# Optimization experiments

Hardware: AMD Instinct MI355X
Metric: run time of the kernel (lower is better)

Reference implementation:

```python
import jax, jax.numpy as jnp
import numpy as np

B, T, HID = 2, 2048, 1536
H, HKV, D = 12, 2, 128
EPS = 1e-6
NEG = -1e9


def setup_inputs() -> dict:
    key = jax.random.key(0)
    ks = jax.random.split(key, 8)
    # rotary embeddings built from real angles (cos/sin of position*inv_freq)
    inv_freq = 1.0 / (10000.0 ** (jnp.arange(0, D, 2, dtype=jnp.float32) / D))  # [D/2]
    pos = jnp.arange(T, dtype=jnp.float32)
    ang = pos[:, None] * inv_freq[None, :]                       # [T, D/2]
    emb = jnp.concatenate([ang, ang], axis=-1)                   # [T, D]
    cos = jnp.broadcast_to(jnp.cos(emb)[None], (B, T, D))
    sin = jnp.broadcast_to(jnp.sin(emb)[None], (B, T, D))
    # additive causal mask [1,1,T,T]
    causal = jnp.tril(jnp.ones((T, T), dtype=bool))
    attention_mask = jnp.where(causal, 0.0, NEG).astype(jnp.float32)[None, None]
    s = 0.02
    return {
        "hidden_states": jax.random.normal(ks[0], (B, T, HID), jnp.float32),
        "cos": cos,
        "sin": sin,
        "attention_mask": attention_mask,
        "q_w": jax.random.normal(ks[1], (H * D, HID), jnp.float32) * s,
        "k_w": jax.random.normal(ks[2], (HKV * D, HID), jnp.float32) * s,
        "v_w": jax.random.normal(ks[3], (HKV * D, HID), jnp.float32) * s,
        "o_w": jax.random.normal(ks[4], (HID, H * D), jnp.float32) * s,
        "q_norm_w": jnp.ones((D,), jnp.float32),
        "k_norm_w": jnp.ones((D,), jnp.float32),
    }


def _rms_norm(x, w):
    # per-head RMSNorm over last dim (head_dim), computed in fp32
    xf = x.astype(jnp.float32)
    var = jnp.mean(xf * xf, axis=-1, keepdims=True)
    return (w * (xf * jax.lax.rsqrt(var + EPS))).astype(x.dtype)


def _rotate_half(x):
    x1, x2 = jnp.split(x, 2, axis=-1)
    return jnp.concatenate([-x2, x1], axis=-1)


def reference(hidden_states, cos, sin, attention_mask, q_w, k_w, v_w, o_w, q_norm_w, k_norm_w):
    b, t, _ = hidden_states.shape
    n_rep = H // HKV
    scale = D ** -0.5

    # projections -> [B, n_heads, T, D]
    q = (hidden_states @ q_w.T).reshape(b, t, H, D)
    k = (hidden_states @ k_w.T).reshape(b, t, HKV, D)
    v = (hidden_states @ v_w.T).reshape(b, t, HKV, D).transpose(0, 2, 1, 3)

    # per-head QK RMSNorm, then to [B, H, T, D]
    q = _rms_norm(q, q_norm_w).transpose(0, 2, 1, 3)
    k = _rms_norm(k, k_norm_w).transpose(0, 2, 1, 3)

    # RoPE (cos/sin broadcast over head axis)
    c = cos[:, None, :, :]
    s = sin[:, None, :, :]
    q = q * c + _rotate_half(q) * s
    k = k * c + _rotate_half(k) * s

    # GQA repeat_kv: [B, HKV, T, D] -> [B, H, T, D]
    k = jnp.repeat(k, n_rep, axis=1)
    v = jnp.repeat(v, n_rep, axis=1)

    attn = jnp.einsum('bhqd,bhkd->bhqk', q, k) * scale + attention_mask
    attn = jax.nn.softmax(attn.astype(jnp.float32), axis=-1).astype(q.dtype)
    out = jnp.einsum('bhqk,bhkd->bhqd', attn, v)
    out = out.transpose(0, 2, 1, 3).reshape(b, t, H * D)
    return out @ o_w.T
```

## Files before the change

kernel.cpp:

```cpp
#include <hip/hip_runtime.h>
#include <hip/hip_bf16.h>


#define B_   2
#define T_   2048
#define HID_ 1536
#define H_   12
#define HKV_ 2
#define D_   128
#define GQ_  (H_ / HKV_)
#define NQKV_ 2048
#define SCALE_ 0.08838834764831845f

typedef unsigned short u16;
typedef __attribute__((ext_vector_type(4))) float f32x4;
typedef __attribute__((ext_vector_type(8))) short bf16x8;
typedef __attribute__((ext_vector_type(4))) unsigned short u16x4;
typedef __attribute__((ext_vector_type(8))) unsigned short u16x8;

__device__ __forceinline__ u16 f2b(float f) {
  union { __hip_bfloat16 h; u16 u; } cv;
  cv.h = __float2bfloat16(f);
  return cv.u;
}
__device__ __forceinline__ float b2f(u16 u) {
  union { float f; unsigned i; } cv;
  cv.i = ((unsigned)u) << 16;
  return cv.f;
}

__device__ __forceinline__ void glds16(const u16* g, u16* l) {
  __builtin_amdgcn_global_load_lds((const __attribute__((address_space(1))) void*)g,
                                   (__attribute__((address_space(3))) void*)l, 16, 0, 0);
}

__global__ __launch_bounds__(256) void cvt_f32_bf16(const float* __restrict__ src,
                                                    u16* __restrict__ dst, int n4) {
  int i = blockIdx.x * 256 + threadIdx.x;
  const int stride = gridDim.x * 256;
  for (; i < n4; i += stride) {
    const float4 v = reinterpret_cast<const float4*>(src)[i];
    u16x4 o = {f2b(v.x), f2b(v.y), f2b(v.z), f2b(v.w)};
    reinterpret_cast<u16x4*>(dst)[i] = o;
  }
}

__device__ __forceinline__ void cstore(float* p, float v) { *p = v; }
__device__ __forceinline__ void cstore(u16* p, float v) { *p = f2b(v); }

template <typename CT>
__global__ __launch_bounds__(256) void gemm_bt(const u16* __restrict__ A,
                                               const u16* __restrict__ W,
                                               CT* __restrict__ C,
                                               int M, int N, int K) {
  __shared__ __align__(16) u16 As[128 * 32];
  __shared__ __align__(16) u16 Ws[128 * 32];
  const int tid  = threadIdx.x;
  const int lane = tid & 63;
  const int wid  = tid >> 6;
  const int wr = wid >> 1, wc = wid & 1;
  const int l15 = lane & 15, kg = lane >> 4;
  const int rowBase = blockIdx.y * 128;
  const int colBase = blockIdx.x * 128;

  const int srow = lane >> 2;
  const int scol = (lane & 3) << 3;
  const u16* Ab = A + (size_t)(rowBase + wid * 16 + srow) * K + scol;
  const u16* Wb = W + (size_t)(colBase + wid * 16 + srow) * K + scol;
  u16* AsW = &As[wid * 512];
  u16* WsW = &Ws[wid * 512];

  const f32x4 zero4 = {0.f, 0.f, 0.f, 0.f};
  f32x4 acc[4][4];
#pragma unroll
  for (int m = 0; m < 4; ++m)
#pragma unroll
    for (int n = 0; n < 4; ++n) acc[m][n] = zero4;

  for (int k0 = 0; k0 < K; k0 += 32) {
    __syncthreads();
    glds16(Ab + k0, AsW);
    glds16(Ab + (size_t)64 * K + k0, AsW + 2048);
    glds16(Wb + k0, WsW);
    glds16(Wb + (size_t)64 * K + k0, WsW + 2048);
    __syncthreads();
    bf16x8 a[4], b[4];
#pragma unroll
    for (int m = 0; m < 4; ++m)
      a[m] = *reinterpret_cast<const bf16x8*>(&As[(wr * 64 + m * 16 + l15) * 32 + kg * 8]);
#pragma unroll
    for (int n = 0; n < 4; ++n)
      b[n] = *reinterpret_cast<const bf16x8*>(&Ws[(wc * 64 + n * 16 + l15) * 32 + kg * 8]);
#pragma unroll
    for (int m = 0; m < 4; ++m)
#pragma unroll
      for (int n = 0; n < 4; ++n)
        acc[m][n] = __builtin_amdgcn_mfma_f32_16x16x32_bf16(a[m], b[n], acc[m][n], 0, 0, 0);
  }
#pragma unroll
  for (int m = 0; m < 4; ++m) {
    const int row0 = rowBase + wr * 64 + m * 16 + kg * 4;
#pragma unroll
    for (int n = 0; n < 4; ++n) {
      const int col = colBase + wc * 64 + n * 16 + l15;
#pragma unroll
      for (int r = 0; r < 4; ++r) cstore(&C[(size_t)(row0 + r) * N + col], acc[m][n][r]);
    }
  }
}

__global__ __launch_bounds__(256) void norm_rope_cvt(
    const u16* __restrict__ qkv, const float* __restrict__ cosb,
    const float* __restrict__ sinb, const float* __restrict__ q_nw,
    const float* __restrict__ k_nw, u16* __restrict__ q_b,
    u16* __restrict__ k_b, u16* __restrict__ vt_b) {
  const int gwave = (int)((blockIdx.x * 256 + threadIdx.x) >> 6);
  const int lane = threadIdx.x & 63;
  const int NQ = B_ * T_ * H_;
  const int NK = B_ * T_ * HKV_;
  if (gwave < NQ) {
    const int bt = gwave / H_, h = gwave - bt * H_;
    const u16* src = qkv + (size_t)bt * NQKV_ + h * D_;
    const float x1 = b2f(src[lane]), x2 = b2f(src[lane + 64]);
    float ss = x1 * x1 + x2 * x2;
#pragma unroll
    for (int m = 32; m >= 1; m >>= 1) ss += __shfl_xor(ss, m);
    const float rinv = rsqrtf(ss * (1.0f / D_) + 1e-6f);
    const float c1 = cosb[(size_t)bt * D_ + lane], c2 = cosb[(size_t)bt * D_ + lane + 64];
    const float s1 = sinb[(size_t)bt * D_ + lane], s2 = sinb[(size_t)bt * D_ + lane + 64];
    const float n1 = x1 * rinv * q_nw[lane], n2 = x2 * rinv * q_nw[lane + 64];
    const float o1 = (n1 * c1 - n2 * s1) * SCALE_;
    const float o2 = (n2 * c2 + n1 * s2) * SCALE_;
    const int b = bt >> 11, t = bt & (T_ - 1);
    u16* dst = q_b + ((size_t)(b * H_ + h) * T_ + t) * D_;
    dst[lane] = f2b(o1);
    dst[lane + 64] = f2b(o2);
  } else if (gwave < NQ + NK) {
    const int r = gwave - NQ;
    const int bt = r >> 1, hv = r & 1;
    const u16* src = qkv + (size_t)bt * NQKV_ + 1536 + hv * D_;
    const float x1 = b2f(src[lane]), x2 = b2f(src[lane + 64]);
    float ss = x1 * x1 + x2 * x2;
#pragma unroll
    for (int m = 32; m >= 1; m >>= 1) ss += __shfl_xor(ss, m);
    const float rinv = rsqrtf(ss * (1.0f / D_) + 1e-6f);
    const float c1 = cosb[(size_t)bt * D_ + lane], c2 = cosb[(size_t)bt * D_ + lane + 64];
    const float s1 = sinb[(size_t)bt * D_ + lane], s2 = sinb[(size_t)bt * D_ + lane + 64];
    const float n1 = x1 * rinv * k_nw[lane], n2 = x2 * rinv * k_nw[lane + 64];
    const float o1 = n1 * c1 - n2 * s1;
    const float o2 = n2 * c2 + n1 * s2;
    const int b = bt >> 11, t = bt & (T_ - 1);
    u16* dst = k_b + ((size_t)(b * HKV_ + hv) * T_ + t) * D_;
    dst[lane] = f2b(o1);
    dst[lane + 64] = f2b(o2);
  } else {
    const int r = gwave - NQ - NK;
    const int bt = r >> 1, hv = r & 1;
    const u16* src = qkv + (size_t)bt * NQKV_ + 1792 + hv * D_;
    const float x1 = b2f(src[lane]), x2 = b2f(src[lane + 64]);
    const int b = bt >> 11, t = bt & (T_ - 1);
    const int kk = t & 63;
    const int tp = (t & ~63) | (kk & 32) | (((kk >> 2) & 3) << 3) |
                   (((kk >> 4) & 1) << 2) | (kk & 3);
    u16* dst = vt_b + (size_t)(b * HKV_ + hv) * D_ * T_;
    dst[(size_t)lane * T_ + tp] = f2b(x1);
    dst[(size_t)(lane + 64) * T_ + tp] = f2b(x2);
  }
}

__global__ __launch_bounds__(256) void attn_kernel(const u16* __restrict__ q_b,
                                                   const u16* __restrict__ k_b,
                                                   const u16* __restrict__ vt_b,
                                                   u16* __restrict__ aout,
                                                   u16* __restrict__ po0,
                                                   float2* __restrict__ ml) {
  __shared__ __align__(16) u16 Ks[64 * 128];
  __shared__ __align__(16) u16 Vs[128 * 64];
  const int bh = blockIdx.x;
  const int y = blockIdx.y;
  const int item = (y & 1) ? (23 - (y >> 1)) : (y >> 1);
  int qt, s, kt0, ktend;
  bool splitq;
  if (item < 8) {
    qt = item; s = 0; kt0 = 0; ktend = 2 * qt + 1; splitq = false;
  } else if (item < 16) {
    qt = item; s = 0; kt0 = 0; ktend = qt; splitq = true;
  } else {
    qt = item - 8; s = 1; kt0 = qt + 1; ktend = 2 * qt + 1; splitq = true;
  }
  const int b = bh / H_, h = bh - b * H_;
  const int kvh = h / GQ_;
  const int tid = threadIdx.x;
  const int w = tid >> 6, lane = tid & 63;
  const int l15 = lane & 15, kg = lane >> 4;
  const int qbase = qt * 128;

  const u16* Kb = k_b + (size_t)(b * HKV_ + kvh) * T_ * D_;
  const u16* Vb = vt_b + (size_t)(b * HKV_ + kvh) * D_ * T_;

  bf16x8 qf[2][4];
#pragma unroll
  for (int qb = 0; qb < 2; ++qb) {
    const u16* qrow =
        q_b + ((size_t)(b * H_ + h) * T_ + qbase + w * 32 + qb * 16 + l15) * D_;
#pragma unroll
    for (int s4 = 0; s4 < 4; ++s4)
      qf[qb][s4] = *reinterpret_cast<const bf16x8*>(qrow + s4 * 32 + kg * 8);
  }

  int kK[4], vK[4];
#pragma unroll
  for (int c = 0; c < 4; ++c) {
    const int ch = w * 4 + c;
    const int kr = ch * 4 + (lane >> 4);
    kK[c] = kr * D_ + (((lane & 15) << 3) ^ ((kr & 7) << 3));
    const int dr = ch * 8 + (lane >> 3);
    vK[c] = dr * T_ + (((lane & 7) << 3) ^ ((dr & 7) << 3));
  }

  const int xorv = (l15 & 7) << 3;

  const f32x4 zero4 = {0.f, 0.f, 0.f, 0.f};
  f32x4 o[2][8];
#pragma unroll
  for (int qb = 0; qb < 2; ++qb)
#pragma unroll
    for (int n = 0; n < 8; ++n) o[qb][n] = zero4;
  float m[2] = {0.f, 0.f};
  float lsum[2] = {0.f, 0.f};

  for (int kt = kt0; kt <= ktend; ++kt) {
    __syncthreads();
    {
      const size_t kb = (size_t)kt * 64;
#pragma unroll
      for (int c = 0; c < 4; ++c) {
        glds16(Kb + kb * D_ + kK[c], &Ks[(w * 4 + c) * 512]);
        glds16(Vb + kb + vK[c], &Vs[(w * 4 + c) * 512]);
      }
    }
    __syncthreads();
    f32x4 sc[2][4];
#pragma unroll
    for (int qb = 0; qb < 2; ++qb)
#pragma unroll
      for (int n = 0; n < 4; ++n) sc[qb][n] = zero4;
#pragma unroll
    for (int n = 0; n < 4; ++n)
#pragma unroll
      for (int s4 = 0; s4 < 4; ++s4) {
        const int koff = (n * 16 + l15) * 128 + ((s4 * 32 + kg * 8) ^ xorv);
        bf16x8 kf = *reinterpret_cast<const bf16x8*>(&Ks[koff]);
#pragma unroll
        for (int qb = 0; qb < 2; ++qb)
          sc[qb][n] = __builtin_amdgcn_mfma_f32_16x16x32_bf16(kf, qf[qb][s4],
                                                              sc[qb][n], 0, 0, 0);
      }
    if (kt >= 2 * qt) {
#pragma unroll
      for (int qb = 0; qb < 2; ++qb) {
        const int qg = w * 32 + qb * 16 + l15;
        const int kbb = (kt - 2 * qt) * 64;
#pragma unroll
        for (int n = 0; n < 4; ++n)
#pragma unroll
          for (int r = 0; r < 4; ++r)
            if (kbb + n * 16 + kg * 4 + r > qg) sc[qb][n][r] = -3e38f;
      }
    }
    float pm[2];
#pragma unroll
    for (int qb = 0; qb < 2; ++qb) {
      float v = sc[qb][0][0];
#pragma unroll
      for (int n = 0; n < 4; ++n)
#pragma unroll
        for (int r = 0; r < 4; ++r) v = fmaxf(v, sc[qb][n][r]);
      v = fmaxf(v, __shfl_xor(v, 16));
      v = fmaxf(v, __shfl_xor(v, 32));
      pm[qb] = v;
    }
    if (__any((pm[0] > m[0] + 8.f) | (pm[1] > m[1] + 8.f))) {
#pragma unroll
      for (int qb = 0; qb < 2; ++qb) {
        const float mn = fmaxf(m[qb], pm[qb]);
        const float al = __expf(m[qb] - mn);
        m[qb] = mn;
        lsum[qb] *= al;
        float alT[4];
#pragma unroll
        for (int r = 0; r < 4; ++r)
          alT[r] = __shfl(al, (lane & 48) | (kg * 4 + r));
#pragma unroll
        for (int n = 0; n < 8; ++n)
#pragma unroll
          for (int r = 0; r < 4; ++r) o[qb][n][r] *= alT[r];
      }
    }
#pragma unroll
    for (int qb = 0; qb < 2; ++qb) {
      float rs = 0.f;
#pragma unroll
      for (int n = 0; n < 4; ++n)
#pragma unroll
        for (int r = 0; r < 4; ++r) {
          const float p = __expf(sc[qb][n][r] - m[qb]);
          sc[qb][n][r] = p;
          rs += p;
        }
      rs += __shfl_xor(rs, 16);
      rs += __shfl_xor(rs, 32);
      lsum[qb] += rs;
    }
    bf16x8 pf[2][2];
#pragma unroll
    for (int qb = 0; qb < 2; ++qb)
#pragma unroll
      for (int ks = 0; ks < 2; ++ks)
#pragma unroll
        for (int r = 0; r < 4; ++r) {
          pf[qb][ks][r] = (short)f2b(sc[qb][2 * ks][r]);
          pf[qb][ks][r + 4] = (short)f2b(sc[qb][2 * ks + 1][r]);
        }
#pragma unroll
    for (int n = 0; n < 8; ++n)
#pragma unroll
      for (int ks = 0; ks < 2; ++ks) {
        const int voff = (n * 16 + l15) * 64 + ((ks * 32 + kg * 8) ^ xorv);
        bf16x8 vf = *reinterpret_cast<const bf16x8*>(&Vs[voff]);
#pragma unroll
        for (int qb = 0; qb < 2; ++qb)
          o[qb][n] = __builtin_amdgcn_mfma_f32_16x16x32_bf16(pf[qb][ks], vf,
                                                             o[qb][n], 0, 0, 0);
      }
  }

  if (!splitq) {
    float invT[2][4];
#pragma unroll
    for (int qb = 0; qb < 2; ++qb) {
      const float inv = 1.0f / lsum[qb];
#pragma unroll
      for (int r = 0; r < 4; ++r)
        invT[qb][r] = __shfl(inv, (lane & 48) | (kg * 4 + r));
    }
#pragma unroll
    for (int qb = 0; qb < 2; ++qb) {
      const int t0 = qbase + w * 32 + qb * 16 + kg * 4;
#pragma unroll
      for (int n = 0; n < 8; ++n)
#pragma unroll
        for (int r = 0; r < 4; ++r)
          aout[(size_t)(b * T_ + t0 + r) * (H_ * D_) + h * D_ + n * 16 + l15] =
              f2b(o[qb][n][r] * invT[qb][r]);
    }
  } else {
    const int slot = bh * 8 + (qt - 8);
    if (kg == 0) {
#pragma unroll
      for (int qb = 0; qb < 2; ++qb) {
        float2 v;
        v.x = m[qb];
        v.y = lsum[qb];
        ml[(size_t)(slot * 2 + s) * 128 + w * 32 + qb * 16 + l15] = v;
      }
    }
    if (s == 1) {
#pragma unroll
      for (int qb = 0; qb < 2; ++qb) {
        const int t0 = qbase + w * 32 + qb * 16 + kg * 4;
#pragma unroll
        for (int n = 0; n < 8; ++n)
#pragma unroll
          for (int r = 0; r < 4; ++r)
            aout[(size_t)(b * T_ + t0 + r) * (H_ * D_) + h * D_ + n * 16 + l15] =
                f2b(o[qb][n][r]);
      }
    } else {
#pragma unroll
      for (int qb = 0; qb < 2; ++qb) {
        const int row0 = w * 32 + qb * 16 + kg * 4;
#pragma unroll
        for (int n = 0; n < 8; ++n)
#pragma unroll
          for (int r = 0; r < 4; ++r)
            po0[((size_t)slot * 128 + row0 + r) * 128 + n * 16 + l15] =
                f2b(o[qb][n][r]);
      }
    }
  }
}

__global__ __launch_bounds__(256) void combine_kernel(u16* __restrict__ aout,
                                                      const u16* __restrict__ po0,
                                                      const float2* __restrict__ ml) {
  const int bh = blockIdx.x;
  const int qt8 = blockIdx.y;
  const int slot = bh * 8 + qt8;
  const int b = bh / H_, h = bh - b * H_;
  const int t0 = (qt8 + 8) * 128;
  const int tid = threadIdx.x;
  const int row = tid >> 1;
  const int colc = (tid & 1) << 6;

  const float2 ml0 = ml[(size_t)(slot * 2 + 0) * 128 + row];
  const float2 ml1 = ml[(size_t)(slot * 2 + 1) * 128 + row];
  const float mm = fmaxf(ml0.x, ml1.x);
  const float c0 = __expf(ml0.x - mm), c1 = __expf(ml1.x - mm);
  const float inv = 1.0f / (ml0.y * c0 + ml1.y * c1);
  const float s0 = c0 * inv, s1 = c1 * inv;

  const u16* p0 = po0 + ((size_t)slot * 128 + row) * 128 + colc;
  u16* a = aout + (size_t)(b * T_ + t0 + row) * (H_ * D_) + h * D_ + colc;
#pragma unroll
  for (int j = 0; j < 8; ++j) {
    u16x8 v0 = *reinterpret_cast<const u16x8*>(p0 + j * 8);
    u16x8 v1 = *reinterpret_cast<const u16x8*>(a + j * 8);
    u16x8 outv;
#pragma unroll
    for (int e = 0; e < 8; ++e) outv[e] = f2b(b2f(v0[e]) * s0 + b2f(v1[e]) * s1);
    *reinterpret_cast<u16x8*>(a + j * 8) = outv;
  }
}

extern "C" void kernel_launch(void* const* d_in, const int* in_sizes, int n_in,
                              void* d_out, int out_size, void* d_ws, size_t ws_size,
                              hipStream_t stream) {
  const float* hidden = (const float*)d_in[0];
  const float* cosb   = (const float*)d_in[1];
  const float* sinb   = (const float*)d_in[2];
  const float* q_w  = (const float*)d_in[4];
  const float* k_w  = (const float*)d_in[5];
  const float* v_w  = (const float*)d_in[6];
  const float* o_w  = (const float*)d_in[7];
  const float* q_nw = (const float*)d_in[8];
  const float* k_nw = (const float*)d_in[9];
  float* out = (float*)d_out;

  char* ws = (char*)d_ws;
  const size_t MB = 1u << 20;
  u16*    hidden_b = (u16*)(ws);
  u16*    qkvw     = (u16*)(ws + 12 * MB);
  u16*    q_b      = (u16*)(ws);
  u16*    aout     = (u16*)(ws + 12 * MB);
  float2* ml       = (float2*)(ws + 24 * MB);
  u16*    k_b      = (u16*)(ws + 24 * MB + 512 * 1024);
  u16*    vt_b     = (u16*)(ws + 26 * MB + 512 * 1024);
  u16*    owb      = (u16*)(ws + 28 * MB + 512 * 1024);
  u16*    qkv_proj = (u16*)d_out;
  u16*    po0      = (u16*)d_out;

  const dim3 blk(256);
  const int M = B_ * T_;

  {
    const int nh = (B_ * T_ * HID_) / 4;
    const int nq = (H_ * D_ * HID_) / 4;
    const int nk = (HKV_ * D_ * HID_) / 4;
    cvt_f32_bf16<<<2048, blk, 0, stream>>>(hidden, hidden_b, nh);
    cvt_f32_bf16<<<2048, blk, 0, stream>>>(q_w, qkvw, nq);
    cvt_f32_bf16<<<384, blk, 0, stream>>>(k_w, qkvw + (size_t)1536 * HID_, nk);
    cvt_f32_bf16<<<384, blk, 0, stream>>>(v_w, qkvw + (size_t)1792 * HID_, nk);
    cvt_f32_bf16<<<2048, blk, 0, stream>>>(o_w, owb, nq);
  }

  gemm_bt<u16><<<dim3(NQKV_ / 128, M / 128), blk, 0, stream>>>(hidden_b, qkvw, qkv_proj,
                                                               M, NQKV_, HID_);

  norm_rope_cvt<<<16384, blk, 0, stream>>>(qkv_proj, cosb, sinb, q_nw, k_nw,
                                           q_b, k_b, vt_b);

  attn_kernel<<<dim3(B_ * H_, 24), blk, 0, stream>>>(q_b, k_b, vt_b, aout, po0, ml);
  combine_kernel<<<dim3(B_ * H_, 8), blk, 0, stream>>>(aout, po0, ml);

  gemm_bt<float><<<dim3(HID_ / 128, M / 128), blk, 0, stream>>>(aout, owb, out,
                                                                M, HID_, HID_);
}
```

Baseline: 197.4 us.

## Rebalance causal attention with variable KV splits and longest-first work ordering

```diff
diff --git a/kernel.cpp b/kernel.cpp
--- a/kernel.cpp
+++ b/kernel.cpp
@@ -168,6 +168,22 @@
   }
 }
 
+__constant__ int QT_ARR[40] = {15,15,15,15,14,14,11,11,11,10, 7, 7, 3,
+                               14,14,13,13,13,13,12,12,10,10, 9, 9, 6, 6,
+                               12,12, 9, 8, 8, 8, 5, 5, 2,
+                                4, 4, 1, 0};
+__constant__ int C_ARR[40]  = { 0, 1, 2, 3, 0, 1, 0, 1, 2, 0, 0, 1,-1,
+                                2, 3, 0, 1, 2, 3, 0, 1, 1, 2, 0, 1, 0, 1,
+                                2, 3, 2, 0, 1, 2, 0, 1,-1,
+                                0, 1,-1,-1};
+__device__ __forceinline__ int nc_of(int qt) { return (qt < 8) ? 2 : ((qt < 12) ? 3 : 4); }
+__device__ __forceinline__ int mlbase_of(int qt) {
+  return (qt < 8) ? 2 * (qt - 4) : ((qt < 12) ? 8 + 3 * (qt - 8) : 20 + 4 * (qt - 12));
+}
+__device__ __forceinline__ int pbase_of(int qt) {
+  return (qt < 8) ? (qt - 4) : ((qt < 12) ? 4 + 2 * (qt - 8) : 12 + 3 * (qt - 12));
+}
+
 __global__ __launch_bounds__(256) void attn_kernel(const u16* __restrict__ q_b,
                                                    const u16* __restrict__ k_b,
                                                    const u16* __restrict__ vt_b,
@@ -176,17 +192,22 @@
                                                    float2* __restrict__ ml) {
   __shared__ __align__(16) u16 Ks[64 * 128];
   __shared__ __align__(16) u16 Vs[128 * 64];
-  const int bh = blockIdx.x;
-  const int y = blockIdx.y;
-  const int item = (y & 1) ? (23 - (y >> 1)) : (y >> 1);
-  int qt, s, kt0, ktend;
-  bool splitq;
-  if (item < 8) {
-    qt = item; s = 0; kt0 = 0; ktend = 2 * qt + 1; splitq = false;
-  } else if (item < 16) {
-    qt = item; s = 0; kt0 = 0; ktend = qt; splitq = true;
+  const int id = blockIdx.x;
+  const int item = id / 24;
+  const int bh = id - item * 24;
+  const int qt = QT_ARR[item];
+  const int c = C_ARR[item];
+  int kt0, ktend;
+  bool partial;
+  if (c < 0) {
+    kt0 = 0; ktend = 2 * qt + 1; partial = false;
   } else {
-    qt = item - 8; s = 1; kt0 = qt + 1; ktend = 2 * qt + 1; splitq = true;
+    const int nt = 2 * qt + 2;
+    const int nc = nc_of(qt);
+    const int base = nt / nc, rem = nt - base * nc;
+    kt0 = c * base + (c < rem ? c : rem);
+    ktend = kt0 + base + (c < rem ? 1 : 0) - 1;
+    partial = true;
   }
   const int b = bh / H_, h = bh - b * H_;
   const int kvh = h / GQ_;
@@ -210,12 +231,12 @@
 
   int kK[4], vK[4];
 #pragma unroll
-  for (int c = 0; c < 4; ++c) {
-    const int ch = w * 4 + c;
+  for (int cc = 0; cc < 4; ++cc) {
+    const int ch = w * 4 + cc;
     const int kr = ch * 4 + (lane >> 4);
-    kK[c] = kr * D_ + (((lane & 15) << 3) ^ ((kr & 7) << 3));
+    kK[cc] = kr * D_ + (((lane & 15) << 3) ^ ((kr & 7) << 3));
     const int dr = ch * 8 + (lane >> 3);
-    vK[c] = dr * T_ + (((lane & 7) << 3) ^ ((dr & 7) << 3));
+    vK[cc] = dr * T_ + (((lane & 7) << 3) ^ ((dr & 7) << 3));
   }
 
   const int xorv = (l15 & 7) << 3;
@@ -234,9 +255,9 @@
     {
       const size_t kb = (size_t)kt * 64;
 #pragma unroll
-      for (int c = 0; c < 4; ++c) {
-        glds16(Kb + kb * D_ + kK[c], &Ks[(w * 4 + c) * 512]);
-        glds16(Vb + kb + vK[c], &Vs[(w * 4 + c) * 512]);
+      for (int cc = 0; cc < 4; ++cc) {
+        glds16(Kb + kb * D_ + kK[cc], &Ks[(w * 4 + cc) * 512]);
+        glds16(Vb + kb + vK[cc], &Vs[(w * 4 + cc) * 512]);
       }
     }
     __syncthreads();
@@ -245,6 +266,7 @@
     for (int qb = 0; qb < 2; ++qb)
 #pragma unroll
       for (int n = 0; n < 4; ++n) sc[qb][n] = zero4;
+    __builtin_amdgcn_s_setprio(1);
 #pragma unroll
     for (int n = 0; n < 4; ++n)
 #pragma unroll
@@ -256,6 +278,7 @@
           sc[qb][n] = __builtin_amdgcn_mfma_f32_16x16x32_bf16(kf, qf[qb][s4],
                                                               sc[qb][n], 0, 0, 0);
       }
+    __builtin_amdgcn_s_setprio(0);
     if (kt >= 2 * qt) {
 #pragma unroll
       for (int qb = 0; qb < 2; ++qb) {
@@ -322,6 +345,7 @@
           pf[qb][ks][r] = (short)f2b(sc[qb][2 * ks][r]);
           pf[qb][ks][r + 4] = (short)f2b(sc[qb][2 * ks + 1][r]);
         }
+    __builtin_amdgcn_s_setprio(1);
 #pragma unroll
     for (int n = 0; n < 8; ++n)
 #pragma unroll
@@ -333,9 +357,10 @@
           o[qb][n] = __builtin_amdgcn_mfma_f32_16x16x32_bf16(pf[qb][ks], vf,
                                                              o[qb][n], 0, 0, 0);
       }
-  }
-
-  if (!splitq) {
+    __builtin_amdgcn_s_setprio(0);
+  }
+
+  if (!partial) {
     float invT[2][4];
 #pragma unroll
     for (int qb = 0; qb < 2; ++qb) {
@@ -355,17 +380,17 @@
               f2b(o[qb][n][r] * invT[qb][r]);
     }
   } else {
-    const int slot = bh * 8 + (qt - 8);
+    const int mlslot = bh * 36 + mlbase_of(qt) + c;
     if (kg == 0) {
 #pragma unroll
       for (int qb = 0; qb < 2; ++qb) {
         float2 v;
         v.x = m[qb];
         v.y = lsum[qb];
-        ml[(size_t)(slot * 2 + s) * 128 + w * 32 + qb * 16 + l15] = v;
-      }
-    }
-    if (s == 1) {
+        ml[(size_t)mlslot * 128 + w * 32 + qb * 16 + l15] = v;
+      }
+    }
+    if (c == 0) {
 #pragma unroll
       for (int qb = 0; qb < 2; ++qb) {
         const int t0 = qbase + w * 32 + qb * 16 + kg * 4;
@@ -377,6 +402,7 @@
                 f2b(o[qb][n][r]);
       }
     } else {
+      const int pslot = bh * 24 + pbase_of(qt) + (c - 1);
 #pragma unroll
       for (int qb = 0; qb < 2; ++qb) {
         const int row0 = w * 32 + qb * 16 + kg * 4;
@@ -384,7 +410,7 @@
         for (int n = 0; n < 8; ++n)
 #pragma unroll
           for (int r = 0; r < 4; ++r)
-            po0[((size_t)slot * 128 + row0 + r) * 128 + n * 16 + l15] =
+            po0[((size_t)pslot * 128 + row0 + r) * 128 + n * 16 + l15] =
                 f2b(o[qb][n][r]);
       }
     }
@@ -394,31 +420,49 @@
 __global__ __launch_bounds__(256) void combine_kernel(u16* __restrict__ aout,
                                                       const u16* __restrict__ po0,
                                                       const float2* __restrict__ ml) {
-  const int bh = blockIdx.x;
-  const int qt8 = blockIdx.y;
-  const int slot = bh * 8 + qt8;
+  const int qt = 4 + blockIdx.x;
+  const int bh = blockIdx.y;
+  const int nc = nc_of(qt);
+  const int mlb = bh * 36 + mlbase_of(qt);
+  const int pb = bh * 24 + pbase_of(qt);
   const int b = bh / H_, h = bh - b * H_;
-  const int t0 = (qt8 + 8) * 128;
+  const int t0 = qt * 128;
   const int tid = threadIdx.x;
   const int row = tid >> 1;
   const int colc = (tid & 1) << 6;
 
-  const float2 ml0 = ml[(size_t)(slot * 2 + 0) * 128 + row];
-  const float2 ml1 = ml[(size_t)(slot * 2 + 1) * 128 + row];
-  const float mm = fmaxf(ml0.x, ml1.x);
-  const float c0 = __expf(ml0.x - mm), c1 = __expf(ml1.x - mm);
-  const float inv = 1.0f / (ml0.y * c0 + ml1.y * c1);
-  const float s0 = c0 * inv, s1 = c1 * inv;
-
-  const u16* p0 = po0 + ((size_t)slot * 128 + row) * 128 + colc;
+  float ms[4], ls[4];
+  float mm = -3e38f;
+  for (int cc = 0; cc < nc; ++cc) {
+    const float2 v = ml[(size_t)(mlb + cc) * 128 + row];
+    ms[cc] = v.x; ls[cc] = v.y;
+    mm = fmaxf(mm, v.x);
+  }
+  float lt = 0.f;
+  float scl[4];
+  for (int cc = 0; cc < nc; ++cc) {
+    scl[cc] = __expf(ms[cc] - mm);
+    lt += ls[cc] * scl[cc];
+  }
+  const float inv = 1.0f / lt;
+  for (int cc = 0; cc < nc; ++cc) scl[cc] *= inv;
+
   u16* a = aout + (size_t)(b * T_ + t0 + row) * (H_ * D_) + h * D_ + colc;
 #pragma unroll
   for (int j = 0; j < 8; ++j) {
-    u16x8 v0 = *reinterpret_cast<const u16x8*>(p0 + j * 8);
-    u16x8 v1 = *reinterpret_cast<const u16x8*>(a + j * 8);
+    u16x8 v0 = *reinterpret_cast<const u16x8*>(a + j * 8);
+    float acc[8];
+#pragma unroll
+    for (int e = 0; e < 8; ++e) acc[e] = b2f(v0[e]) * scl[0];
+    for (int cc = 1; cc < nc; ++cc) {
+      const u16* p = po0 + ((size_t)(pb + cc - 1) * 128 + row) * 128 + colc;
+      u16x8 vc = *reinterpret_cast<const u16x8*>(p + j * 8);
+#pragma unroll
+      for (int e = 0; e < 8; ++e) acc[e] += b2f(vc[e]) * scl[cc];
+    }
     u16x8 outv;
 #pragma unroll
-    for (int e = 0; e < 8; ++e) outv[e] = f2b(b2f(v0[e]) * s0 + b2f(v1[e]) * s1);
+    for (int e = 0; e < 8; ++e) outv[e] = f2b(acc[e]);
     *reinterpret_cast<u16x8*>(a + j * 8) = outv;
   }
 }
@@ -444,9 +488,9 @@
   u16*    q_b      = (u16*)(ws);
   u16*    aout     = (u16*)(ws + 12 * MB);
   float2* ml       = (float2*)(ws + 24 * MB);
-  u16*    k_b      = (u16*)(ws + 24 * MB + 512 * 1024);
-  u16*    vt_b     = (u16*)(ws + 26 * MB + 512 * 1024);
-  u16*    owb      = (u16*)(ws + 28 * MB + 512 * 1024);
+  u16*    k_b      = (u16*)(ws + 25 * MB);
+  u16*    vt_b     = (u16*)(ws + 27 * MB);
+  u16*    owb      = (u16*)(ws + 29 * MB);
   u16*    qkv_proj = (u16*)d_out;
   u16*    po0      = (u16*)d_out;
 
@@ -470,8 +514,8 @@
   norm_rope_cvt<<<16384, blk, 0, stream>>>(qkv_proj, cosb, sinb, q_nw, k_nw,
                                            q_b, k_b, vt_b);
 
-  attn_kernel<<<dim3(B_ * H_, 24), blk, 0, stream>>>(q_b, k_b, vt_b, aout, po0, ml);
-  combine_kernel<<<dim3(B_ * H_, 8), blk, 0, stream>>>(aout, po0, ml);
+  attn_kernel<<<960, blk, 0, stream>>>(q_b, k_b, vt_b, aout, po0, ml);
+  combine_kernel<<<dim3(12, B_ * H_), blk, 0, stream>>>(aout, po0, ml);
 
   gemm_bt<float><<<dim3(HID_ / 128, M / 128), blk, 0, stream>>>(aout, owb, out,
                                                                 M, HID_, HID_);
```

Result: slower. 211.0 us (+6.9%).
